# Kernel tuning notes

Measured on AMD Instinct MI355X. Metric: run time of the kernel, lower is better.

The kernel has to match this reference:

```python
import jax, jax.numpy as jnp
import numpy as np

B, T, K = 512, 1024, 48          # batch, seq_len, n_tokens
START, END = 46, 47              # token_dict['START'], token_dict['END']
NEG = -10000.0


def setup_inputs() -> dict:
    key = jax.random.key(0)
    k1, k2 = jax.random.split(key)
    feats = jax.random.normal(k1, (B, T, K), dtype=jnp.float32)
    transitions = jax.random.normal(k2, (K, K), dtype=jnp.float32)
    return {"feats": feats, "transitions": transitions}


def _mask_transitions(transitions):
    # Mirrors __init__: no transition out of END-column target / into START row.
    t = transitions.at[START, :].set(NEG)
    t = t.at[:, END].set(NEG)
    return t


def _crf_logz(feats, trans):
    """forward_prop: CRF forward algorithm. feats [T,K], trans [K_next,K_prev]."""
    init = jnp.full((K,), NEG, feats.dtype).at[START].set(0.0)

    def step(alpha, feat):
        # scores[next, prev] = alpha[prev] + trans[next, prev] + feat[next]
        scores = alpha[None, :] + trans + feat[:, None]
        return jax.nn.logsumexp(scores, axis=1), None

    alpha, _ = jax.lax.scan(step, init, feats)
    return jax.nn.logsumexp(alpha + trans[END])


def _viterbi(feats, trans):
    """viterbi_decode: max-product recurrence + backtrace. feats [T,K]."""
    init = jnp.full((K,), NEG, feats.dtype).at[START].set(0.0)

    def step(v, feat):
        # NOTE: original takes argmax BEFORE adding emission, then adds feat.
        scores = v[None, :] + trans          # [K_next, K_prev]
        bp = jnp.argmax(scores, axis=1)      # backpointers [K]
        return jnp.max(scores, axis=1) + feat, bp

    v, bptrs = jax.lax.scan(step, init, feats)   # bptrs [T, K]
    term = v + trans[END]
    last = jnp.argmax(term)
    path_score = term[last]

    def back(tag, bp):
        return bp[tag], tag

    _, path = jax.lax.scan(back, last, bptrs, reverse=True)  # path [T]
    return path_score, path


def reference(feats, transitions):
    trans = _mask_transitions(transitions)
    logz = jax.vmap(lambda f: _crf_logz(f, trans))(feats)          # [B]
    scores, paths = jax.vmap(lambda f: _viterbi(f, trans))(feats)  # [B], [B,T]
    return logz, scores, paths
```

## Files before the change

### kernel.cpp

```cpp
#include <hip/hip_runtime.h>

#define NB 512
#define NT 1024
#define NK 48
#define NEGV -10000.0f
#define S_START 46
#define S_END 47
#define NCH 64
#define CLEN 16

__device__ __forceinline__ float rfl_f32(float x) {
    return __int_as_float(__builtin_amdgcn_readfirstlane(__float_as_int(x)));
}

extern "C" __global__ __launch_bounds__(256, 1)
void crf_fused(const float* __restrict__ feats, const float* __restrict__ trans,
               float* __restrict__ out)
{
    __shared__ unsigned char bp[NT * NK];
    __shared__ float ckpt[4 * NK];
    __shared__ unsigned char comp[NCH * NK];
    __shared__ unsigned char boundary[NCH];
    __shared__ float eabuf[64];
    __shared__ float vbuf1[64];
    __shared__ float vbufw[2][64];

    const int b = blockIdx.x;
    const int wave = threadIdx.x >> 6;
    const int lane = threadIdx.x & 63;
    const bool act = lane < NK;
    const int LL = act ? lane : (NK - 1);
    const float* f = feats + (size_t)b * NT * NK;
    const float* fb = f + LL;

    float tEnd = NEGV;
    if (act && lane != S_END) tEnd = trans[S_END * NK + lane];

    if (wave == 0) {
        float Erow[NK];
        {
            const bool rowdead = (lane == S_START);
            const float4* r4 = (const float4*)(trans + LL * NK);
            #pragma unroll
            for (int q = 0; q < NK / 4; ++q) {
                float4 r = r4[q];
                const int c = 4 * q;
                Erow[c + 0] = (rowdead || c + 0 == S_END) ? 0.0f : __expf(r.x);
                Erow[c + 1] = (rowdead || c + 1 == S_END) ? 0.0f : __expf(r.y);
                Erow[c + 2] = (rowdead || c + 2 == S_END) ? 0.0f : __expf(r.z);
                Erow[c + 3] = (rowdead || c + 3 == S_END) ? 0.0f : __expf(r.w);
            }
        }
        float u = (lane == S_START) ? 0.0f : NEGV;
        float Muni = 0.0f;
        eabuf[lane] = __expf(u);
        __builtin_amdgcn_wave_barrier();
        float fr0 = fb[0 * NK], fr1 = fb[1 * NK], fr2 = fb[2 * NK], fr3 = fb[3 * NK];

        auto fstep = [&](float fc) {
            float ea[NK];
            {
                const float4* e4 = (const float4*)eabuf;
                #pragma unroll
                for (int q = 0; q < NK / 4; ++q) {
                    float4 r = e4[q];
                    ea[4 * q + 0] = r.x; ea[4 * q + 1] = r.y;
                    ea[4 * q + 2] = r.z; ea[4 * q + 3] = r.w;
                }
            }
            float a0 = 0.f, a1 = 0.f, a2 = 0.f, a3 = 0.f;
            #pragma unroll
            for (int p = 0; p < NK; p += 4) {
                a0 = fmaf(Erow[p + 0], ea[p + 0], a0);
                a1 = fmaf(Erow[p + 1], ea[p + 1], a1);
                a2 = fmaf(Erow[p + 2], ea[p + 2], a2);
                a3 = fmaf(Erow[p + 3], ea[p + 3], a3);
            }
            float acc = (a0 + a1) + (a2 + a3);
            float w = __logf(acc) + fc;
            float dM = rfl_f32(w);
            Muni += dM;
            u = w - dM;
            __builtin_amdgcn_wave_barrier();
            eabuf[lane] = __expf(u);
            __builtin_amdgcn_wave_barrier();
        };

        __syncthreads();
        for (int it = 0; it <= NCH; ++it) {
            if (it < NCH) {
                #pragma unroll
                for (int g = 0; g < 4; ++g) {
                    const int t = it * CLEN + 4 * g;
                    { float fc = fr0; int nr = (t + 4 < NT) ? t + 4 : NT - 1; fr0 = fb[nr * NK]; fstep(fc); }
                    { float fc = fr1; int nr = (t + 5 < NT) ? t + 5 : NT - 1; fr1 = fb[nr * NK]; fstep(fc); }
                    { float fc = fr2; int nr = (t + 6 < NT) ? t + 6 : NT - 1; fr2 = fb[nr * NK]; fstep(fc); }
                    { float fc = fr3; int nr = (t + 7 < NT) ? t + 7 : NT - 1; fr3 = fb[nr * NK]; fstep(fc); }
                }
            }
            __syncthreads();
        }
        float x = act ? (u + tEnd) : -INFINITY;
        float M2 = x;
        #pragma unroll
        for (int off = 32; off >= 1; off >>= 1)
            M2 = fmaxf(M2, __shfl_xor(M2, off, 64));
        float e = __expf(x - M2);
        #pragma unroll
        for (int off = 32; off >= 1; off >>= 1)
            e += __shfl_xor(e, off, 64);
        if (lane == 0) out[b] = Muni + M2 + __logf(e);
    } else if (wave == 1) {
        float trow[NK];
        {
            const bool rowdead = (lane == S_START);
            const float4* r4 = (const float4*)(trans + LL * NK);
            #pragma unroll
            for (int q = 0; q < NK / 4; ++q) {
                float4 r = r4[q];
                const int c = 4 * q;
                trow[c + 0] = (rowdead || c + 0 == S_END) ? NEGV : r.x;
                trow[c + 1] = (rowdead || c + 1 == S_END) ? NEGV : r.y;
                trow[c + 2] = (rowdead || c + 2 == S_END) ? NEGV : r.z;
                trow[c + 3] = (rowdead || c + 3 == S_END) ? NEGV : r.w;
            }
        }
        float v = (lane == S_START) ? 0.0f : NEGV;
        vbuf1[lane] = v;
        if (act) ckpt[0 * NK + lane] = v;
        __builtin_amdgcn_wave_barrier();
        float fr0 = fb[0 * NK], fr1 = fb[1 * NK], fr2 = fb[2 * NK], fr3 = fb[3 * NK];

        auto vstep = [&](float fc) {
            float s[NK];
            {
                const float4* v4 = (const float4*)vbuf1;
                #pragma unroll
                for (int q = 0; q < NK / 4; ++q) {
                    float4 r = v4[q];
                    s[4 * q + 0] = r.x + trow[4 * q + 0];
                    s[4 * q + 1] = r.y + trow[4 * q + 1];
                    s[4 * q + 2] = r.z + trow[4 * q + 2];
                    s[4 * q + 3] = r.w + trow[4 * q + 3];
                }
            }
            float m16[16];
            #pragma unroll
            for (int i = 0; i < 16; ++i)
                m16[i] = fmaxf(fmaxf(s[3 * i], s[3 * i + 1]), s[3 * i + 2]);
            float m6[6];
            #pragma unroll
            for (int i = 0; i < 5; ++i)
                m6[i] = fmaxf(fmaxf(m16[3 * i], m16[3 * i + 1]), m16[3 * i + 2]);
            m6[5] = m16[15];
            float best = fmaxf(fmaxf(fmaxf(m6[0], m6[1]), m6[2]),
                               fmaxf(fmaxf(m6[3], m6[4]), m6[5]));
            v = best + fc;
            __builtin_amdgcn_wave_barrier();
            vbuf1[lane] = v;
            __builtin_amdgcn_wave_barrier();
        };

        int last = 0;
        __syncthreads();
        for (int it = 0; it <= NCH; ++it) {
            if (it < NCH) {
                #pragma unroll
                for (int g = 0; g < 4; ++g) {
                    const int t = it * CLEN + 4 * g;
                    { float fc = fr0; int nr = (t + 4 < NT) ? t + 4 : NT - 1; fr0 = fb[nr * NK]; vstep(fc); }
                    { float fc = fr1; int nr = (t + 5 < NT) ? t + 5 : NT - 1; fr1 = fb[nr * NK]; vstep(fc); }
                    { float fc = fr2; int nr = (t + 6 < NT) ? t + 6 : NT - 1; fr2 = fb[nr * NK]; vstep(fc); }
                    { float fc = fr3; int nr = (t + 7 < NT) ? t + 7 : NT - 1; fr3 = fb[nr * NK]; vstep(fc); }
                }
                if (act && it + 1 < NCH) ckpt[((it + 1) & 3) * NK + lane] = v;
            } else {
                float xv = act ? (v + tEnd) : -INFINITY;
                int idx = act ? lane : 63;
                float val = xv;
                #pragma unroll
                for (int off = 32; off >= 1; off >>= 1) {
                    float ov = __shfl_xor(val, off, 64);
                    int   oi = __shfl_xor(idx, off, 64);
                    if (ov > val || (ov == val && oi < idx)) { val = ov; idx = oi; }
                }
                if (lane == 0) out[NB + b] = val;
                last = idx;
            }
            __syncthreads();
        }
        if (lane == 0) {
            int tag = last;
            for (int l = NCH - 1; l >= 0; --l) {
                boundary[l] = (unsigned char)tag;
                tag = comp[l * NK + tag];
            }
        }
        __builtin_amdgcn_wave_barrier();
        int tag = boundary[lane];
        float* pout = out + 2 * NB + (size_t)b * NT;
        const int tbase = lane * CLEN;
        for (int i = CLEN - 1; i >= 0; --i) {
            pout[tbase + i] = (float)tag;
            tag = bp[(tbase + i) * NK + tag];
        }
    } else {
        const int w = wave - 2;
        float trow[NK];
        {
            const bool rowdead = (lane == S_START);
            const float4* r4 = (const float4*)(trans + LL * NK);
            #pragma unroll
            for (int q = 0; q < NK / 4; ++q) {
                float4 r = r4[q];
                const int c = 4 * q;
                trow[c + 0] = (rowdead || c + 0 == S_END) ? NEGV : r.x;
                trow[c + 1] = (rowdead || c + 1 == S_END) ? NEGV : r.y;
                trow[c + 2] = (rowdead || c + 2 == S_END) ? NEGV : r.z;
                trow[c + 3] = (rowdead || c + 3 == S_END) ? NEGV : r.w;
            }
        }
        float* vbw = vbufw[w];
        const int big = 63;
        int bpl[8], bph[8];

        auto replay8 = [&](int c, int base, int* bparr8) {
            const float* fbc = fb + (size_t)c * CLEN * NK;
            unsigned char* bpc = bp + (size_t)c * CLEN * NK;
            float fv[8];
            #pragma unroll
            for (int i = 0; i < 8; ++i) fv[i] = fbc[(base + i) * NK];
            #pragma unroll
            for (int i = 0; i < 8; ++i) {
                float s[NK];
                {
                    const float4* v4 = (const float4*)vbw;
                    #pragma unroll
                    for (int q = 0; q < NK / 4; ++q) {
                        float4 r = v4[q];
                        s[4 * q + 0] = r.x + trow[4 * q + 0];
                        s[4 * q + 1] = r.y + trow[4 * q + 1];
                        s[4 * q + 2] = r.z + trow[4 * q + 2];
                        s[4 * q + 3] = r.w + trow[4 * q + 3];
                    }
                }
                float m16[16];
                #pragma unroll
                for (int j = 0; j < 16; ++j)
                    m16[j] = fmaxf(fmaxf(s[3 * j], s[3 * j + 1]), s[3 * j + 2]);
                float m6[6];
                #pragma unroll
                for (int j = 0; j < 5; ++j)
                    m6[j] = fmaxf(fmaxf(m16[3 * j], m16[3 * j + 1]), m16[3 * j + 2]);
                m6[5] = m16[15];
                float best = fmaxf(fmaxf(fmaxf(m6[0], m6[1]), m6[2]),
                                   fmaxf(fmaxf(m6[3], m6[4]), m6[5]));
                int n16[16];
                #pragma unroll
                for (int j = 0; j < 16; ++j) {
                    int r = (s[3 * j + 2] == best) ? 3 * j + 2 : big;
                    r = (s[3 * j + 1] == best) ? 3 * j + 1 : r;
                    r = (s[3 * j + 0] == best) ? 3 * j + 0 : r;
                    n16[j] = r;
                }
                int n6[6];
                #pragma unroll
                for (int j = 0; j < 5; ++j)
                    n6[j] = min(min(n16[3 * j], n16[3 * j + 1]), n16[3 * j + 2]);
                n6[5] = n16[15];
                int bi = min(min(min(n6[0], n6[1]), n6[2]),
                             min(min(n6[3], n6[4]), n6[5]));

                bparr8[i] = bi;
                bpc[(base + i) * NK + LL] = (unsigned char)bi;
                float vn = best + fv[i];
                __builtin_amdgcn_wave_barrier();
                vbw[lane] = vn;
                __builtin_amdgcn_wave_barrier();
            }
        };

        __syncthreads();
        for (int it = 0; it <= NCH; ++it) {
            if ((it & 1) == w && it < NCH) {
                vbw[lane] = ckpt[(it & 3) * NK + LL];
                __builtin_amdgcn_wave_barrier();
                replay8(it, 0, bpl);
            } else if ((it & 1) != w && it >= 1) {
                const int c = it - 1;
                replay8(c, 8, bph);
                int tag = act ? lane : 0;
                #pragma unroll
                for (int i = 7; i >= 0; --i)
                    tag = __builtin_amdgcn_ds_bpermute(tag << 2, bph[i]);
                #pragma unroll
                for (int i = 7; i >= 0; --i)
                    tag = __builtin_amdgcn_ds_bpermute(tag << 2, bpl[i]);
                if (act) comp[c * NK + lane] = (unsigned char)tag;
            }
            __syncthreads();
        }
    }
}

extern "C" void kernel_launch(void* const* d_in, const int* in_sizes, int n_in,
                              void* d_out, int out_size, void* d_ws, size_t ws_size,
                              hipStream_t stream) {
    (void)in_sizes; (void)n_in; (void)d_ws; (void)ws_size; (void)out_size;
    const float* feats = (const float*)d_in[0];
    const float* trans = (const float*)d_in[1];
    float* out = (float*)d_out;
    crf_fused<<<dim3(NB), dim3(256), 0, stream>>>(feats, trans, out);
}
```

Measured before the change: 493.9 us.

## Keep CRF forward in linear space with exponent renormalization; double chunk length

The forward recurrence now stays in probability space. Each step multiplies by exp(feat) and renormalizes by the power of two taken from lane 0's exponent bits, which drops the per-step log/exp pair in favour of a single exp and integer exponent tracking. Chunk length grows from 16 to 32, halving the number of block-wide barriers, and replay waves now process 16 steps per half. Wave roles are also rotated by block index to spread roles across SIMDs. Risks include underflow from renormalizing on lane 0 only, and higher register pressure from the 16-entry backpointer arrays.

```diff
diff --git a/kernel.cpp b/kernel.cpp
--- a/kernel.cpp
+++ b/kernel.cpp
@@ -6,8 +6,8 @@
 #define NEGV -10000.0f
 #define S_START 46
 #define S_END 47
-#define NCH 64
-#define CLEN 16
+#define NCH 32
+#define CLEN 32
 
 __device__ __forceinline__ float rfl_f32(float x) {
     return __int_as_float(__builtin_amdgcn_readfirstlane(__float_as_int(x)));
@@ -27,6 +27,7 @@
 
     const int b = blockIdx.x;
     const int wave = threadIdx.x >> 6;
+    const int role = (wave + b) & 3;
     const int lane = threadIdx.x & 63;
     const bool act = lane < NK;
     const int LL = act ? lane : (NK - 1);
@@ -36,7 +37,7 @@
     float tEnd = NEGV;
     if (act && lane != S_END) tEnd = trans[S_END * NK + lane];
 
-    if (wave == 0) {
+    if (role == 0) {
         float Erow[NK];
         {
             const bool rowdead = (lane == S_START);
@@ -51,46 +52,48 @@
                 Erow[c + 3] = (rowdead || c + 3 == S_END) ? 0.0f : __expf(r.w);
             }
         }
-        float u = (lane == S_START) ? 0.0f : NEGV;
-        float Muni = 0.0f;
-        eabuf[lane] = __expf(u);
+        float ea = (lane == S_START) ? 1.0f : 0.0f;
+        int Etot = 0;
+        eabuf[lane] = ea;
         __builtin_amdgcn_wave_barrier();
         float fr0 = fb[0 * NK], fr1 = fb[1 * NK], fr2 = fb[2 * NK], fr3 = fb[3 * NK];
 
         auto fstep = [&](float fc) {
-            float ea[NK];
+            float ef = __expf(fc);
+            float eav[NK];
             {
                 const float4* e4 = (const float4*)eabuf;
                 #pragma unroll
                 for (int q = 0; q < NK / 4; ++q) {
                     float4 r = e4[q];
-                    ea[4 * q + 0] = r.x; ea[4 * q + 1] = r.y;
-                    ea[4 * q + 2] = r.z; ea[4 * q + 3] = r.w;
+                    eav[4 * q + 0] = r.x; eav[4 * q + 1] = r.y;
+                    eav[4 * q + 2] = r.z; eav[4 * q + 3] = r.w;
                 }
             }
             float a0 = 0.f, a1 = 0.f, a2 = 0.f, a3 = 0.f;
             #pragma unroll
             for (int p = 0; p < NK; p += 4) {
-                a0 = fmaf(Erow[p + 0], ea[p + 0], a0);
-                a1 = fmaf(Erow[p + 1], ea[p + 1], a1);
-                a2 = fmaf(Erow[p + 2], ea[p + 2], a2);
-                a3 = fmaf(Erow[p + 3], ea[p + 3], a3);
+                a0 = fmaf(Erow[p + 0], eav[p + 0], a0);
+                a1 = fmaf(Erow[p + 1], eav[p + 1], a1);
+                a2 = fmaf(Erow[p + 2], eav[p + 2], a2);
+                a3 = fmaf(Erow[p + 3], eav[p + 3], a3);
             }
             float acc = (a0 + a1) + (a2 + a3);
-            float w = __logf(acc) + fc;
-            float dM = rfl_f32(w);
-            Muni += dM;
-            u = w - dM;
+            float nv = acc * ef;
+            float nvr = rfl_f32(nv);
+            int e = ((__float_as_int(nvr) >> 23) & 255) - 127;
+            Etot += e;
+            float sc = __int_as_float((127 - e) << 23);
+            ea = nv * sc;
             __builtin_amdgcn_wave_barrier();
-            eabuf[lane] = __expf(u);
+            eabuf[lane] = ea;
             __builtin_amdgcn_wave_barrier();
         };
 
         __syncthreads();
         for (int it = 0; it <= NCH; ++it) {
             if (it < NCH) {
-                #pragma unroll
-                for (int g = 0; g < 4; ++g) {
+                for (int g = 0; g < CLEN / 4; ++g) {
                     const int t = it * CLEN + 4 * g;
                     { float fc = fr0; int nr = (t + 4 < NT) ? t + 4 : NT - 1; fr0 = fb[nr * NK]; fstep(fc); }
                     { float fc = fr1; int nr = (t + 5 < NT) ? t + 5 : NT - 1; fr1 = fb[nr * NK]; fstep(fc); }
@@ -100,17 +103,19 @@
             }
             __syncthreads();
         }
+        float u = __logf(ea);
         float x = act ? (u + tEnd) : -INFINITY;
         float M2 = x;
         #pragma unroll
         for (int off = 32; off >= 1; off >>= 1)
             M2 = fmaxf(M2, __shfl_xor(M2, off, 64));
-        float e = __expf(x - M2);
+        float es = __expf(x - M2);
         #pragma unroll
         for (int off = 32; off >= 1; off >>= 1)
-            e += __shfl_xor(e, off, 64);
-        if (lane == 0) out[b] = Muni + M2 + __logf(e);
-    } else if (wave == 1) {
+            es += __shfl_xor(es, off, 64);
+        if (lane == 0)
+            out[b] = (float)Etot * 0.6931471805599453f + M2 + __logf(es);
+    } else if (role == 1) {
         float trow[NK];
         {
             const bool rowdead = (lane == S_START);
@@ -165,8 +170,7 @@
         __syncthreads();
         for (int it = 0; it <= NCH; ++it) {
             if (it < NCH) {
-                #pragma unroll
-                for (int g = 0; g < 4; ++g) {
+                for (int g = 0; g < CLEN / 4; ++g) {
                     const int t = it * CLEN + 4 * g;
                     { float fc = fr0; int nr = (t + 4 < NT) ? t + 4 : NT - 1; fr0 = fb[nr * NK]; vstep(fc); }
                     { float fc = fr1; int nr = (t + 5 < NT) ? t + 5 : NT - 1; fr1 = fb[nr * NK]; vstep(fc); }
@@ -197,15 +201,17 @@
             }
         }
         __builtin_amdgcn_wave_barrier();
-        int tag = boundary[lane];
-        float* pout = out + 2 * NB + (size_t)b * NT;
-        const int tbase = lane * CLEN;
-        for (int i = CLEN - 1; i >= 0; --i) {
-            pout[tbase + i] = (float)tag;
-            tag = bp[(tbase + i) * NK + tag];
+        if (lane < NCH) {
+            int tag = boundary[lane];
+            float* pout = out + 2 * NB + (size_t)b * NT;
+            const int tbase = lane * CLEN;
+            for (int i = CLEN - 1; i >= 0; --i) {
+                pout[tbase + i] = (float)tag;
+                tag = bp[(tbase + i) * NK + tag];
+            }
         }
     } else {
-        const int w = wave - 2;
+        const int w = role - 2;
         float trow[NK];
         {
             const bool rowdead = (lane == S_START);
@@ -222,16 +228,16 @@
         }
         float* vbw = vbufw[w];
         const int big = 63;
-        int bpl[8], bph[8];
-
-        auto replay8 = [&](int c, int base, int* bparr8) {
+        int bpl[16], bph[16];
+
+        auto replay16 = [&](int c, int base, int* ba) {
             const float* fbc = fb + (size_t)c * CLEN * NK;
             unsigned char* bpc = bp + (size_t)c * CLEN * NK;
-            float fv[8];
-            #pragma unroll
-            for (int i = 0; i < 8; ++i) fv[i] = fbc[(base + i) * NK];
-            #pragma unroll
-            for (int i = 0; i < 8; ++i) {
+            float fv[16];
+            #pragma unroll
+            for (int i = 0; i < 16; ++i) fv[i] = fbc[(base + i) * NK];
+            #pragma unroll
+            for (int i = 0; i < 16; ++i) {
                 float s[NK];
                 {
                     const float4* v4 = (const float4*)vbw;
@@ -271,7 +277,7 @@
                 int bi = min(min(min(n6[0], n6[1]), n6[2]),
                              min(min(n6[3], n6[4]), n6[5]));
 
-                bparr8[i] = bi;
+                ba[i] = bi;
                 bpc[(base + i) * NK + LL] = (unsigned char)bi;
                 float vn = best + fv[i];
                 __builtin_amdgcn_wave_barrier();
@@ -282,19 +288,19 @@
 
         __syncthreads();
         for (int it = 0; it <= NCH; ++it) {
-            if ((it & 1) == w && it < NCH) {
+            if (it < NCH && (it & 1) == w) {
                 vbw[lane] = ckpt[(it & 3) * NK + LL];
                 __builtin_amdgcn_wave_barrier();
-                replay8(it, 0, bpl);
-            } else if ((it & 1) != w && it >= 1) {
+                replay16(it, 0, bpl);
+            } else if (it >= 1 && ((it - 1) & 1) == w) {
                 const int c = it - 1;
-                replay8(c, 8, bph);
+                replay16(c, 16, bph);
                 int tag = act ? lane : 0;
                 #pragma unroll
-                for (int i = 7; i >= 0; --i)
+                for (int i = 15; i >= 0; --i)
                     tag = __builtin_amdgcn_ds_bpermute(tag << 2, bph[i]);
                 #pragma unroll
-                for (int i = 7; i >= 0; --i)
+                for (int i = 15; i >= 0; --i)
                     tag = __builtin_amdgcn_ds_bpermute(tag << 2, bpl[i]);
                 if (act) comp[c * NK + lane] = (unsigned char)tag;
             }
```

Result: no change. 484.4 us (-1.9%).
